# Kernel tuning notes

Measured on AMD Instinct MI355X. Metric: run time of the kernel, lower is better.

## Reference

```python
import jax, jax.numpy as jnp
import numpy as np

HEADS = 16

def setup_inputs() -> dict:
    key = jax.random.key(0)
    ks = jax.random.split(key, 4)
    emb = 1024
    x = jax.random.normal(ks[0], (2, 2048, emb), dtype=jnp.float32)
    Wqkv = jax.random.normal(ks[1], (emb, 3 * emb), dtype=jnp.float32) * 0.02
    bqkv = jnp.zeros((3 * emb,), dtype=jnp.float32)
    Wproj = jax.random.normal(ks[2], (emb, emb), dtype=jnp.float32) * 0.02
    bproj = jnp.zeros((emb,), dtype=jnp.float32)
    return {"x": x, "Wqkv": Wqkv, "bqkv": bqkv, "Wproj": Wproj, "bproj": bproj}


def reference(x, Wqkv, bqkv, Wproj, bproj):
    b, n, e = x.shape
    h = HEADS
    d = e // h
    # qkv projection; last dim factors as (h, d, 3): q/k/v interleaved innermost,
    # matching einops rearrange 'b n (h d q) -> q b h n d'
    t = (x @ Wqkv + bqkv).reshape(b, n, h, d, 3)
    q, k, v = t[..., 0], t[..., 1], t[..., 2]  # each [b, n, h, d]
    scale = np.float32(1.0 / np.sqrt(e))  # note: sqrt(emb), not sqrt(head_dim)
    att = jax.nn.softmax(jnp.einsum('bnhd,bmhd->bhnm', q, k) * scale, axis=-1)
    out = jnp.einsum('bhnm,bmhd->bnhd', att, v).reshape(b, n, e)
    return out @ Wproj + bproj
```

## Files before the change

### kernel.cpp

```cpp
#include <hip/hip_runtime.h>

typedef __bf16 bf16;
typedef __attribute__((ext_vector_type(8))) __bf16 bf16x8;
typedef __attribute__((ext_vector_type(4))) float f32x4;
typedef __attribute__((ext_vector_type(16))) float f32x16;
typedef unsigned int u32;
typedef __attribute__((ext_vector_type(2))) unsigned int u32x2;
typedef __attribute__((ext_vector_type(4))) unsigned int u32x4;

#define SEQ 2048
#define EMB 1024
#define NH  16
#define DH  64

__global__ __launch_bounds__(256) void prep(const float* __restrict__ x, bf16* __restrict__ xb,
                                            const float* __restrict__ Wqkv, bf16* __restrict__ WqkvT,
                                            const float* __restrict__ Wproj, bf16* __restrict__ WprojT) {
    __shared__ float t[32][33];
    int b = blockIdx.x;
    if (b < 2048) {
        int i = b * 256 + threadIdx.x;
        float4 a = ((const float4*)x)[2 * i];
        float4 c = ((const float4*)x)[2 * i + 1];
        bf16x8 o;
        o[0] = (bf16)a.x; o[1] = (bf16)a.y; o[2] = (bf16)a.z; o[3] = (bf16)a.w;
        o[4] = (bf16)c.x; o[5] = (bf16)c.y; o[6] = (bf16)c.z; o[7] = (bf16)c.w;
        ((bf16x8*)xb)[i] = o;
        return;
    }
    int tx = threadIdx.x & 31, ty = threadIdx.x >> 5;
    if (b < 5120) {
        int flat = b - 2048;
        int c0 = (flat % 96) * 32, r0 = (flat / 96) * 32;
#pragma unroll
        for (int s = 0; s < 4; s++) {
            int row = ty + s * 8;
            t[row][tx] = Wqkv[(size_t)(r0 + row) * 3072 + c0 + tx];
        }
        __syncthreads();
#pragma unroll
        for (int s = 0; s < 4; s++) {
            int row = ty + s * 8;
            int corig = c0 + row;
            int hh = corig / 192;
            int rem = corig - hh * 192;
            int dd = rem / 3;
            int which = rem - dd * 3;
            int colp = which * 1024 + hh * 64 + dd;
            WqkvT[(size_t)colp * EMB + r0 + tx] = (bf16)t[tx][row];
        }
    } else {
        int flat = b - 5120;
        int c0 = (flat % 32) * 32, r0 = (flat / 32) * 32;
#pragma unroll
        for (int s = 0; s < 4; s++) {
            int row = ty + s * 8;
            t[row][tx] = Wproj[(size_t)(r0 + row) * EMB + c0 + tx];
        }
        __syncthreads();
#pragma unroll
        for (int s = 0; s < 4; s++) {
            int row = ty + s * 8;
            WprojT[(size_t)(c0 + row) * EMB + r0 + tx] = (bf16)t[tx][row];
        }
    }
}


#define BM 128
#define BN 128
#define BK 32

__device__ __forceinline__ void gload16(const bf16* g, bf16* l) {
    __builtin_amdgcn_global_load_lds((__attribute__((address_space(1))) void*)(void*)g,
                                     (__attribute__((address_space(3))) void*)l, 16, 0, 0);
}

__device__ __forceinline__ void stage_tile(const bf16* src, int ld, int row0, int k0,
                                           bf16* lds, int wave, int lane) {
#pragma unroll
    for (int c = 0; c < 2; c++) {
        int chunk = wave + 4 * c;
        int row = chunk * 16 + (lane >> 2);
        int slot = (lane & 3) ^ ((lane >> 2) & 3);
        const bf16* g = src + (size_t)(row0 + row) * ld + k0 + slot * 8;
        gload16(g, lds + chunk * 512);
    }
}

__device__ __forceinline__ bf16x8 frag(const bf16* lds, int row, int s) {
    int slot = s ^ (row & 3);
    return *(const bf16x8*)&lds[row * BK + slot * 8];
}

__device__ __forceinline__ void gemm_mainloop(const bf16* A, const bf16* Bt, int Kdim,
                                              int m0, int n0, bf16* As, bf16* Bs,
                                              int wave, int lane, int wr, int wc,
                                              f32x4 acc[4][4]) {
    const int iters = Kdim / BK;
    stage_tile(A, Kdim, m0, 0, As, wave, lane);
    stage_tile(Bt, Kdim, n0, 0, Bs, wave, lane);
    stage_tile(A, Kdim, m0, BK, As + BM * BK, wave, lane);
    stage_tile(Bt, Kdim, n0, BK, Bs + BM * BK, wave, lane);
    asm volatile("s_waitcnt vmcnt(4)" ::: "memory");
    __builtin_amdgcn_s_barrier();

    for (int it = 0; it < iters; ++it) {
        int cur = it % 3;
        bool more = (it + 2 < iters);
        if (more) {
            int nxt = (it + 2) % 3;
            stage_tile(A, Kdim, m0, (it + 2) * BK, As + nxt * BM * BK, wave, lane);
            stage_tile(Bt, Kdim, n0, (it + 2) * BK, Bs + nxt * BM * BK, wave, lane);
        }
        const bf16* as = As + cur * BM * BK;
        const bf16* bs = Bs + cur * BM * BK;
        int s = lane >> 4;
        bf16x8 a[4], b[4];
#pragma unroll
        for (int i = 0; i < 4; i++)
            a[i] = frag(as, wr * 64 + i * 16 + (lane & 15), s);
#pragma unroll
        for (int j = 0; j < 4; j++)
            b[j] = frag(bs, wc * 64 + j * 16 + (lane & 15), s);
#pragma unroll
        for (int i = 0; i < 4; i++)
#pragma unroll
            for (int j = 0; j < 4; j++)
                acc[i][j] = __builtin_amdgcn_mfma_f32_16x16x32_bf16(a[i], b[j], acc[i][j], 0, 0, 0);
        if (more)
            asm volatile("s_waitcnt vmcnt(4)" ::: "memory");
        else
            asm volatile("s_waitcnt vmcnt(0)" ::: "memory");
        __builtin_amdgcn_s_barrier();
    }
}

__global__ __launch_bounds__(256) void gemm_qkv(const bf16* __restrict__ A,
                                                const bf16* __restrict__ Bt,
                                                const float* __restrict__ bias,
                                                bf16* __restrict__ Qb, bf16* __restrict__ Kb,
                                                bf16* __restrict__ Vt) {
    __shared__ alignas(16) bf16 smem[6 * BM * BK];
    bf16* As = smem;
    bf16* Bs = smem + 3 * BM * BK;
    int wave = threadIdx.x >> 6, lane = threadIdx.x & 63;
    int wr = wave >> 1, wc = wave & 1;

    int flat = blockIdx.y * 24 + blockIdx.x;
    int swz = (flat & 7) * 96 + (flat >> 3);
    int n0 = (swz % 24) * BN;
    int m0 = (swz / 24) * BM;

    f32x4 acc[4][4] = {};
    gemm_mainloop(A, Bt, EMB, m0, n0, As, Bs, wave, lane, wr, wc, acc);

    int which = n0 >> 10;
    bool isV = (which == 2);
    char* tile = (char*)smem;
    __builtin_amdgcn_s_barrier();

#pragma unroll
    for (int i = 0; i < 4; i++) {
#pragma unroll
        for (int j = 0; j < 4; j++) {
            int c = wc * 64 + j * 16 + (lane & 15);
            int hh = ((n0 + c) >> 6) & 15;
            int dd = c & 63;
            float bv = bias[hh * 192 + dd * 3 + which];
#pragma unroll
            for (int r = 0; r < 4; r++) {
                int rowL = wr * 64 + i * 16 + 4 * (lane >> 4) + r;
                float v = acc[i][j][r] + bv;
                if (which == 0) v *= 0.03125f;
                int byte;
                if (!isV) byte = rowL * 256 + ((c * 2) ^ ((rowL & 7) << 4));
                else      byte = c * 256 + ((((rowL >> 3) ^ (c & 15)) << 4) + (rowL & 7) * 2);
                *(bf16*)(tile + byte) = (bf16)v;
            }
        }
    }
    __builtin_amdgcn_s_barrier();

    int tid = threadIdx.x;
    if (which == 0) {
#pragma unroll
        for (int k = 0; k < 8; k++) {
            int f = k * 256 + tid;
            int rowL = f >> 4, ch = f & 15;
            bf16x8 val = *(const bf16x8*)(tile + rowL * 256 + ((ch ^ (rowL & 7)) << 4));
            int grow = m0 + rowL;
            int bb = grow >> 11, npos = grow & 2047;
            int cbase = ch * 8;
            int hh = ((n0 + cbase) >> 6) & 15;
            int d0 = cbase & 63;
            *(bf16x8*)(Qb + (((size_t)bb * NH + hh) * SEQ + npos) * DH + d0) = val;
        }
    } else if (which == 1) {
#pragma unroll
        for (int k = 0; k < 8; k++) {
            int f = k * 256 + tid;
            int rowL = f >> 4, ch = f & 15;
            bf16x8 val = *(const bf16x8*)(tile + rowL * 256 + ((ch ^ (rowL & 7)) << 4));
            int grow = m0 + rowL;
            int bb = grow >> 11, npos = grow & 2047;
            int cbase = ch * 8;
            int hh = ((n0 + cbase) >> 6) & 15;
            int d0 = cbase & 63;
            size_t base = ((size_t)bb * NH + hh) * (SEQ * DH) + (size_t)(npos >> 6) * 4096;
            int chunk = ((npos >> 5) & 1) * 8 + (d0 >> 4) * 2 + ((d0 >> 3) & 1);
            *(bf16x8*)(Kb + base + chunk * 256 + (npos & 31) * 8) = val;
        }
    } else {
#pragma unroll
        for (int k = 0; k < 8; k++) {
            int f = k * 256 + tid;
            int cL = f >> 4, g = f & 15;
            bf16x8 val = *(const bf16x8*)(tile + cL * 256 + ((g ^ (cL & 15)) << 4));
            int grow = m0 + g * 8;
            int bb = grow >> 11, nn = grow & 2047;
            int hh = ((n0 + cL) >> 6) & 15;
            int d = cL & 63;
            int tIdx = nn >> 6;
            int mb = nn & 63;
            int mc = mb >> 4, half = (mb >> 3) & 1;
            char* base = (char*)Vt +
                         (((size_t)bb * NH + hh) * (SEQ * DH) + (size_t)tIdx * 4096) * 2;
            u32x4 vv = __builtin_bit_cast(u32x4, val);
            u32x2 lo = {vv.x, vv.y};
            u32x2 hi = {vv.z, vv.w};
            int off = ((d >> 5) * 4 + mc) * 1024 + (d & 31) * 16 + half * 8;
            *(u32x2*)(base + off) = lo;
            *(u32x2*)(base + off + 512) = hi;
        }
    }
}

__global__ __launch_bounds__(256) void gemm_proj(const bf16* __restrict__ A,
                                                 const bf16* __restrict__ Bt,
                                                 const float* __restrict__ bias,
                                                 float* __restrict__ C) {
    __shared__ alignas(16) bf16 smem[6 * BM * BK];
    bf16* As = smem;
    bf16* Bs = smem + 3 * BM * BK;
    int wave = threadIdx.x >> 6, lane = threadIdx.x & 63;
    int wr = wave >> 1, wc = wave & 1;
    int m0 = blockIdx.y * BM, n0 = blockIdx.x * BN;
    f32x4 acc[4][4] = {};
    gemm_mainloop(A, Bt, EMB, m0, n0, As, Bs, wave, lane, wr, wc, acc);

    int m_base = m0 + wr * 64;
    int n_base = n0 + wc * 64;
#pragma unroll
    for (int i = 0; i < 4; i++) {
#pragma unroll
        for (int j = 0; j < 4; j++) {
            int col = n_base + j * 16 + (lane & 15);
            float bv = bias[col];
#pragma unroll
            for (int r = 0; r < 4; r++) {
                int row = m_base + i * 16 + 4 * (lane >> 4) + r;
                C[(size_t)row * EMB + col] = acc[i][j][r] + bv;
            }
        }
    }
}


__device__ __forceinline__ void stage16k(const bf16* src, bf16* lds, int wave, int lane) {
#pragma unroll
    for (int i = 0; i < 4; i++) {
        int c = wave * 4 + i;
        gload16(src + c * 512 + lane * 8, lds + c * 512);
    }
}

__device__ __forceinline__ u32 pack_bf16(float lo, float hi) {
    unsigned short a = __builtin_bit_cast(unsigned short, (bf16)lo);
    unsigned short b = __builtin_bit_cast(unsigned short, (bf16)hi);
    return (u32)a | ((u32)b << 16);
}

__global__ __launch_bounds__(256, 2) void attn(const bf16* __restrict__ Q,
                                               const bf16* __restrict__ K,
                                               const bf16* __restrict__ Vt,
                                               bf16* __restrict__ O) {
    int flat = blockIdx.x;
    int swz = (flat & 7) * 64 + (flat >> 3);
    int bh = swz >> 4;
    int qb = swz & 15;

    int wave = threadIdx.x >> 6, lane = threadIdx.x & 63;
    int l31 = lane & 31, h = lane >> 5;
    int qw0 = qb * 128 + wave * 32;
    const bf16* Qg = Q + (size_t)bh * SEQ * DH;
    const bf16* Kg = K + (size_t)bh * SEQ * DH;
    const bf16* Vg = Vt + (size_t)bh * SEQ * DH;

    __shared__ alignas(16) bf16 Ks[2][8192];
    __shared__ alignas(16) bf16 Vs[2][8192];

    bf16x8 qf[4];
#pragma unroll
    for (int ks = 0; ks < 4; ks++)
        qf[ks] = *(const bf16x8*)(Qg + (size_t)(qw0 + l31) * DH + ks * 16 + h * 8);

    f32x16 Oc[2] = {};
    float lsum = 0.f;

    stage16k(Kg, &Ks[0][0], wave, lane);
    stage16k(Vg, &Vs[0][0], wave, lane);
    asm volatile("s_waitcnt vmcnt(0)" ::: "memory");
    __builtin_amdgcn_s_barrier();

    int cur = 0;
    const int NIT = SEQ / 128;
    for (int it = 0; it < NIT; ++it) {
        if (it + 1 < NIT) {
            stage16k(Kg + (size_t)(it + 1) * 8192, &Ks[cur ^ 1][0], wave, lane);
            stage16k(Vg + (size_t)(it + 1) * 8192, &Vs[cur ^ 1][0], wave, lane);
        }
        const char* kc = (const char*)&Ks[cur][0];
        const char* vc = (const char*)&Vs[cur][0];

        u32 w[4][8];
        float part[4];
#pragma unroll
        for (int T = 0; T < 4; T++) {
            bf16x8 kf[4];
#pragma unroll
            for (int ks = 0; ks < 4; ks++)
                kf[ks] = *(const bf16x8*)(kc + (((T * 4 + ks) * 2 + h) << 9) + l31 * 16);
            f32x16 st = {};
            __builtin_amdgcn_s_setprio(1);
#pragma unroll
            for (int ks = 0; ks < 4; ks++)
                st = __builtin_amdgcn_mfma_f32_32x32x16_bf16(kf[ks], qf[ks], st, 0, 0, 0);
            __builtin_amdgcn_s_setprio(0);
            float acc = 0.f;
#pragma unroll
            for (int p = 0; p < 8; p++) {
                float p0 = __expf(st[2 * p]);
                float p1 = __expf(st[2 * p + 1]);
                acc += p0 + p1;
                w[T][p] = pack_bf16(p0, p1);
            }
            part[T] = acc;
        }
        lsum += (part[0] + part[1]) + (part[2] + part[3]);

        __builtin_amdgcn_s_setprio(1);
#pragma unroll
        for (int mg = 0; mg < 2; mg++)
#pragma unroll
            for (int dt = 0; dt < 2; dt++)
#pragma unroll
                for (int mc = 0; mc < 4; mc++) {
                    bf16x8 vf = *(const bf16x8*)(vc + mg * 8192 +
                                                 (((dt * 4 + mc) * 2 + h) << 9) + l31 * 16);
                    int Tw = mg * 2 + (mc >> 1);
                    u32x4 pw = {w[Tw][4 * (mc & 1) + 0], w[Tw][4 * (mc & 1) + 1],
                                w[Tw][4 * (mc & 1) + 2], w[Tw][4 * (mc & 1) + 3]};
                    bf16x8 pa = __builtin_bit_cast(bf16x8, pw);
                    Oc[dt] = __builtin_amdgcn_mfma_f32_32x32x16_bf16(pa, vf, Oc[dt], 0, 0, 0);
                }
        __builtin_amdgcn_s_setprio(0);

        asm volatile("s_waitcnt vmcnt(0)" ::: "memory");
        __builtin_amdgcn_s_barrier();
        cur ^= 1;
    }

    float ls = lsum + __shfl_xor(lsum, 32);
    float rinv = 1.0f / ls;
    int bb = bh >> 4, hh = bh & 15;
#pragma unroll
    for (int reg = 0; reg < 16; reg++) {
        int qlocal = (reg & 3) + 8 * (reg >> 2) + 4 * h;
        float sc = __shfl(rinv, qlocal);
        int row = qw0 + qlocal;
#pragma unroll
        for (int dt = 0; dt < 2; dt++) {
            O[((size_t)bb * SEQ + row) * EMB + hh * DH + dt * 32 + l31] =
                (bf16)(Oc[dt][reg] * sc);
        }
    }
}


extern "C" void kernel_launch(void* const* d_in, const int* in_sizes, int n_in,
                              void* d_out, int out_size, void* d_ws, size_t ws_size,
                              hipStream_t stream) {
    const float* x     = (const float*)d_in[0];
    const float* Wqkv  = (const float*)d_in[1];
    const float* bqkv  = (const float*)d_in[2];
    const float* Wproj = (const float*)d_in[3];
    const float* bproj = (const float*)d_in[4];
    float* out = (float*)d_out;
    char* ws = (char*)d_ws;

    bf16* xb     = (bf16*)(ws + 0);
    bf16* attO   = xb;
    bf16* WqkvT  = (bf16*)(ws + 8388608);
    bf16* WprojT = (bf16*)(ws + 14680064);
    bf16* Qb     = (bf16*)(ws + 16777216);
    bf16* Kb     = (bf16*)(ws + 25165824);
    bf16* Vt     = (bf16*)(ws + 33554432);

    prep<<<6144, 256, 0, stream>>>(x, xb, Wqkv, WqkvT, Wproj, WprojT);
    gemm_qkv<<<dim3(24, 32), 256, 0, stream>>>(xb, WqkvT, bqkv, Qb, Kb, Vt);
    attn<<<512, 256, 0, stream>>>(Qb, Kb, Vt, attO);
    gemm_proj<<<dim3(8, 32), 256, 0, stream>>>(attO, WprojT, bproj, out);
}
```

Measured before the change: 118.9 us.

## Split attention over key halves with combine pass, read V from global

Splits the attention key range into two halves, doubling the grid to 1024 blocks, and writes unnormalized partial outputs plus row sums to scratch space (the output buffer and the freed WqkvT region). A new combine kernel adds the halves, normalizes, and writes the head-interleaved layout. V is no longer staged in LDS and is read directly from global memory, which halves LDS use and raises launch bounds to 4 blocks per CU. The aim is more parallelism and occupancy, at the cost of an extra kernel launch, a partial-output round trip, and uncached global V loads inside the MFMA loop.

```diff
diff --git a/kernel.cpp b/kernel.cpp
--- a/kernel.cpp
+++ b/kernel.cpp
@@ -281,11 +281,14 @@
     return (u32)a | ((u32)b << 16);
 }
 
-__global__ __launch_bounds__(256, 2) void attn(const bf16* __restrict__ Q,
+__global__ __launch_bounds__(256, 4) void attn(const bf16* __restrict__ Q,
                                                const bf16* __restrict__ K,
                                                const bf16* __restrict__ Vt,
-                                               bf16* __restrict__ O) {
-    int flat = blockIdx.x;
+                                               bf16* __restrict__ Op,
+                                               float* __restrict__ lsumP) {
+    int fl = blockIdx.x;
+    int half = fl >> 9;
+    int flat = fl & 511;
     int swz = (flat & 7) * 64 + (flat >> 3);
     int bh = swz >> 4;
     int qb = swz & 15;
@@ -294,11 +297,10 @@
     int l31 = lane & 31, h = lane >> 5;
     int qw0 = qb * 128 + wave * 32;
     const bf16* Qg = Q + (size_t)bh * SEQ * DH;
-    const bf16* Kg = K + (size_t)bh * SEQ * DH;
-    const bf16* Vg = Vt + (size_t)bh * SEQ * DH;
+    const bf16* Kg = K + (size_t)bh * SEQ * DH + half * 65536;
+    const bf16* Vg = Vt + (size_t)bh * SEQ * DH + half * 65536;
 
     __shared__ alignas(16) bf16 Ks[2][8192];
-    __shared__ alignas(16) bf16 Vs[2][8192];
 
     bf16x8 qf[4];
 #pragma unroll
@@ -309,19 +311,17 @@
     float lsum = 0.f;
 
     stage16k(Kg, &Ks[0][0], wave, lane);
-    stage16k(Vg, &Vs[0][0], wave, lane);
     asm volatile("s_waitcnt vmcnt(0)" ::: "memory");
     __builtin_amdgcn_s_barrier();
 
     int cur = 0;
-    const int NIT = SEQ / 128;
+    const int NIT = 8;
     for (int it = 0; it < NIT; ++it) {
         if (it + 1 < NIT) {
             stage16k(Kg + (size_t)(it + 1) * 8192, &Ks[cur ^ 1][0], wave, lane);
-            stage16k(Vg + (size_t)(it + 1) * 8192, &Vs[cur ^ 1][0], wave, lane);
         }
         const char* kc = (const char*)&Ks[cur][0];
-        const char* vc = (const char*)&Vs[cur][0];
+        const bf16* vgi = Vg + (size_t)it * 8192;
 
         u32 w[4][8];
         float part[4];
@@ -356,8 +356,8 @@
             for (int dt = 0; dt < 2; dt++)
 #pragma unroll
                 for (int mc = 0; mc < 4; mc++) {
-                    bf16x8 vf = *(const bf16x8*)(vc + mg * 8192 +
-                                                 (((dt * 4 + mc) * 2 + h) << 9) + l31 * 16);
+                    bf16x8 vf = *(const bf16x8*)(vgi + mg * 4096 +
+                                                 ((dt * 4 + mc) * 2 + h) * 256 + l31 * 8);
                     int Tw = mg * 2 + (mc >> 1);
                     u32x4 pw = {w[Tw][4 * (mc & 1) + 0], w[Tw][4 * (mc & 1) + 1],
                                 w[Tw][4 * (mc & 1) + 2], w[Tw][4 * (mc & 1) + 3]};
@@ -372,19 +372,36 @@
     }
 
     float ls = lsum + __shfl_xor(lsum, 32);
-    float rinv = 1.0f / ls;
-    int bb = bh >> 4, hh = bh & 15;
+    if (h == 0)
+        lsumP[((size_t)half * 32 + bh) * SEQ + qw0 + l31] = ls;
+
+    bf16* dst = Op + (((size_t)half * 32 + bh) * SEQ + qw0) * DH;
 #pragma unroll
     for (int reg = 0; reg < 16; reg++) {
         int qlocal = (reg & 3) + 8 * (reg >> 2) + 4 * h;
-        float sc = __shfl(rinv, qlocal);
-        int row = qw0 + qlocal;
-#pragma unroll
-        for (int dt = 0; dt < 2; dt++) {
-            O[((size_t)bb * SEQ + row) * EMB + hh * DH + dt * 32 + l31] =
-                (bf16)(Oc[dt][reg] * sc);
-        }
-    }
+#pragma unroll
+        for (int dt = 0; dt < 2; dt++)
+            dst[(size_t)qlocal * DH + dt * 32 + l31] = (bf16)Oc[dt][reg];
+    }
+}
+
+__global__ __launch_bounds__(256) void attn_combine(const bf16* __restrict__ Op,
+                                                    const float* __restrict__ lsumP,
+                                                    bf16* __restrict__ O) {
+    int g = blockIdx.x * 256 + threadIdx.x;
+    int dg = g & 7;
+    int q = (g >> 3) & 2047;
+    int bh = g >> 14;
+    size_t po = ((size_t)bh * SEQ + q) * DH + dg * 8;
+    bf16x8 a = *(const bf16x8*)(Op + po);
+    bf16x8 b = *(const bf16x8*)(Op + (size_t)32 * SEQ * DH + po);
+    float rinv = 1.0f / (lsumP[(size_t)bh * SEQ + q] + lsumP[(size_t)(32 + bh) * SEQ + q]);
+    bf16x8 o;
+#pragma unroll
+    for (int j = 0; j < 8; j++)
+        o[j] = (bf16)(((float)a[j] + (float)b[j]) * rinv);
+    int bb = bh >> 4, hh = bh & 15;
+    *(bf16x8*)(O + ((size_t)bb * SEQ + q) * EMB + hh * DH + dg * 8) = o;
 }
 
 
@@ -402,13 +419,16 @@
     bf16* xb     = (bf16*)(ws + 0);
     bf16* attO   = xb;
     bf16* WqkvT  = (bf16*)(ws + 8388608);
+    float* lsumP = (float*)(ws + 8388608);
     bf16* WprojT = (bf16*)(ws + 14680064);
     bf16* Qb     = (bf16*)(ws + 16777216);
     bf16* Kb     = (bf16*)(ws + 25165824);
     bf16* Vt     = (bf16*)(ws + 33554432);
+    bf16* Op     = (bf16*)d_out;
 
     prep<<<6144, 256, 0, stream>>>(x, xb, Wqkv, WqkvT, Wproj, WprojT);
     gemm_qkv<<<dim3(24, 32), 256, 0, stream>>>(xb, WqkvT, bqkv, Qb, Kb, Vt);
-    attn<<<512, 256, 0, stream>>>(Qb, Kb, Vt, attO);
+    attn<<<1024, 256, 0, stream>>>(Qb, Kb, Vt, Op, lsumP);
+    attn_combine<<<2048, 256, 0, stream>>>(Op, lsumP, attO);
     gemm_proj<<<dim3(8, 32), 256, 0, stream>>>(attO, WprojT, bproj, out);
 }
```

After: 225.8 us. 89.8% more time.
